# Performance work log

Measured on AMD Instinct MI355X. Metric: run time of the kernel, lower is better.

## Reference

```python
import jax, jax.numpy as jnp
import numpy as np


def setup_inputs() -> dict:
    key = jax.random.key(0)
    ks = jax.random.split(key, 5)
    B, C, S = 4, 64, 96          # batch, in_c, square spatial size
    H = 8                        # num_heads
    x = jax.random.normal(ks[0], (B, C, S, S), dtype=jnp.float32)
    # 1x1 conv weights stored as (out_c, in_c) matrices
    w_vkq = jax.random.normal(ks[1], (3 * H * C, C), dtype=jnp.float32) * 0.02
    b_vkq = jax.random.normal(ks[2], (3 * H * C,), dtype=jnp.float32) * 0.02
    w_out = jax.random.normal(ks[3], (C, C * H), dtype=jnp.float32) * 0.02
    b_out = jax.random.normal(ks[4], (C,), dtype=jnp.float32) * 0.02
    return {"x": x, "w_vkq": w_vkq, "b_vkq": b_vkq, "w_out": w_out, "b_out": b_out}


def reference(x, w_vkq, b_vkq, w_out, b_out):
    B, C, Hh, W = x.shape                       # module requires Hh == W
    H = w_vkq.shape[0] // (3 * C)               # num_heads
    # to_vkq: 1x1 conv == per-pixel matmul over channels -> (B, 3HC, Hh, W)
    vqk = jnp.einsum('bcxy,oc->boxy', x, w_vkq) + b_vkq[None, :, None, None]
    # torch .view reinterprets spatial (Hh, W) flat buffer as (W, Hh)
    vqk = vqk.reshape(B, 3, H, C, W, Hh)
    v, q, k = vqk[:, 0], vqk[:, 1], vqk[:, 2]
    # channel-wise attention: contract over the 'y' axis, keep channel dim
    h = jnp.einsum('bhcxy,bhczy->bhcxz', v, k) / (W * Hh)   # (B,H,C,W,W)
    h = jax.nn.softmax(h, axis=-1)
    h = jnp.einsum('bhcxy,bhczy->bhcxz', h, q)              # (B,H,C,W,W)
    # rearrange 'b h c x y -> b (c h) x y'  (c outer, h inner)
    h = h.transpose(0, 2, 1, 3, 4).reshape(B, C * H, W, W)
    # to_out: 1x1 conv back to in_c channels
    return jnp.einsum('bkxy,ok->boxy', h, w_out) + b_out[None, :, None, None]
```

## Files before the change

kernel.cpp:

```cpp
#include <hip/hip_runtime.h>
#include <cstdint>
#include <cstddef>

typedef float f32x4 __attribute__((ext_vector_type(4)));
typedef float f32x2 __attribute__((ext_vector_type(2)));
typedef __bf16 bf16x8 __attribute__((ext_vector_type(8)));
typedef __bf16 bf16x2 __attribute__((ext_vector_type(2)));
typedef uint32_t u32x4 __attribute__((ext_vector_type(4)));

#define TSS 9216
#define VST 9344
#define VSF 9472
#define KSB 104
#define KST 104
#define XST 72
#define WST 72
#define RSTD 68
#define EPS 68

#define FP8_SCALE 32.0f

__device__ __forceinline__ uint32_t pack2bf(float a, float b) {
  bf16x2 v = { (__bf16)a, (__bf16)b };
  return __builtin_bit_cast(uint32_t, v);
}
__device__ __forceinline__ uint32_t pack4fp8(float a, float b, float c, float d) {
  uint32_t r = __builtin_amdgcn_cvt_pk_fp8_f32(a, b, 0, false);
  return (uint32_t)__builtin_amdgcn_cvt_pk_fp8_f32(c, d, (int)r, true);
}
__device__ __forceinline__ uint2 fp8x4_to_bf16x4_ns(uint32_t v) {
  const f32x2 lo = __builtin_amdgcn_cvt_pk_f32_fp8((int)v, false);
  const f32x2 hi = __builtin_amdgcn_cvt_pk_f32_fp8((int)v, true);
  return uint2{pack2bf(lo[0], lo[1]), pack2bf(hi[0], hi[1])};
}

__global__ __launch_bounds__(256, 8) void wcvt_kernel(
    const float* __restrict__ w, uint16_t* __restrict__ wbf)
{
  const int i = blockIdx.x * 256 + threadIdx.x;
  const float4 v = ((const float4*)w)[i];
  ((uint2*)wbf)[i] = uint2{pack2bf(v.x * FP8_SCALE, v.y * FP8_SCALE),
                           pack2bf(v.z * FP8_SCALE, v.w * FP8_SCALE)};
}

__global__ __launch_bounds__(256, 4) void proj_kernel(
    const float* __restrict__ x, const uint16_t* __restrict__ wbf,
    const float* __restrict__ b_vkq,
    uint8_t* __restrict__ Vr, uint8_t* __restrict__ Qr, uint8_t* __restrict__ Kr)
{
  __shared__ __align__(16) uint16_t Bt[64 * XST];
  __shared__ __align__(16) uint8_t  Ep[4][16 * EPS];

  const int t   = threadIdx.x;
  const int blk = blockIdx.x;
  const int oq  = (blk >> 3) & 3;
  const int bn  = (blk & 7) | ((blk >> 5) << 3);
  const int nt  = bn % 144;
  const int b   = bn / 144;
  const int n0  = nt * 64;

  {
    const float* __restrict__ xb = x + (size_t)b * 64 * TSS + n0;
    const int p  = t & 63;
    const int c0 = (t >> 6) * 16;
    float v[16];
    #pragma unroll
    for (int i = 0; i < 16; ++i) v[i] = xb[(size_t)(c0 + i) * TSS + p];
    #pragma unroll
    for (int h = 0; h < 2; ++h)
      *(uint4*)&Bt[p * XST + c0 + h*8] =
        uint4{pack2bf(v[h*8+0], v[h*8+1]), pack2bf(v[h*8+2], v[h*8+3]),
              pack2bf(v[h*8+4], v[h*8+5]), pack2bf(v[h*8+6], v[h*8+7])};
  }
  __syncthreads();

  const int L    = t & 63;
  const int w    = t >> 6;
  const int lcol = L & 15;
  const int lq   = L >> 4;

  bf16x8 af[4][2];
  #pragma unroll
  for (int tm = 0; tm < 4; ++tm)
    #pragma unroll
    for (int ks = 0; ks < 2; ++ks)
      af[tm][ks] = *(const bf16x8*)&Bt[(tm*16 + lcol) * XST + ks*32 + lq*8];

  const int obase = oq * 384 + w * 96;

  bf16x8 bw[3][2];
  float  bias_r[3];
  #pragma unroll
  for (int pre = 0; pre < 3; ++pre) {
    const int o = obase + pre*16 + lcol;
    #pragma unroll
    for (int ks = 0; ks < 2; ++ks)
      bw[pre][ks] = *(const bf16x8*)(wbf + (size_t)o * 64 + ks*32 + lq*8);
    bias_r[pre] = b_vkq[o] * FP8_SCALE;
  }

  uint8_t* __restrict__ ep = Ep[w];

  #pragma unroll
  for (int ot = 0; ot < 6; ++ot) {
    const int s3   = ot % 3;
    const float bias = bias_r[s3];
    f32x4 acc[4];
    #pragma unroll
    for (int tm = 0; tm < 4; ++tm) acc[tm] = f32x4{bias, bias, bias, bias};
    #pragma unroll
    for (int tm = 0; tm < 4; ++tm)
      #pragma unroll
      for (int ks = 0; ks < 2; ++ks)
        acc[tm] = __builtin_amdgcn_mfma_f32_16x16x32_bf16(af[tm][ks], bw[s3][ks], acc[tm], 0, 0, 0);
    if (ot < 3) {
      const int on = obase + (ot + 3)*16 + lcol;
      #pragma unroll
      for (int ks = 0; ks < 2; ++ks)
        bw[s3][ks] = *(const bf16x8*)(wbf + (size_t)on * 64 + ks*32 + lq*8);
      bias_r[s3] = b_vkq[on] * FP8_SCALE;
    }
    #pragma unroll
    for (int tm = 0; tm < 4; ++tm)
      *(uint32_t*)&ep[lcol * EPS + tm*16 + lq*4] =
        pack4fp8(acc[tm][0], acc[tm][1], acc[tm][2], acc[tm][3]);

    const int o_t  = obase + ot * 16;
    const int sreg = o_t >> 9;
    uint8_t* __restrict__ reg = (sreg == 0) ? Vr : ((sreg == 1) ? Qr : Kr);
    const size_t rb = (size_t)(b * 512 + (o_t & 511)) * VSF + n0;
    #pragma unroll
    for (int s = 0; s < 4; ++s) {
      const int orow = s*4 + lq;
      const uint32_t d = *(const uint32_t*)&ep[orow * EPS + lcol*4];
      *(uint32_t*)(reg + rb + (size_t)orow * VSF + lcol*4) = d;
    }
  }
}

__global__ __launch_bounds__(384, 4) void attn_kernel(
    const uint8_t* __restrict__ Vr, const uint8_t* __restrict__ Qr,
    const uint8_t* __restrict__ Kr, uint16_t* __restrict__ Obuf)
{
  __shared__ __align__(16) uint8_t  KP[96 * 208];
  __shared__ __align__(16) uint16_t Qs[96 * KST];

  const int t   = threadIdx.x;
  const int blk = blockIdx.x;
  const int b   = blk >> 9;
  const int hc  = blk & 511;
  const size_t pb8 = (size_t)(b * 512 + hc) * VSF;
  const uint8_t* __restrict__ vplane = Vr + pb8;

  {
    const uint4* __restrict__ sk = (const uint4*)(Kr + pb8);
    const uint4* __restrict__ sq = (const uint4*)(Qr + pb8);
    #pragma unroll
    for (int half = 0; half < 2; ++half) {
      const int g = t + half * 384;
      if (half == 0 || t < 192) {
        const int row = g / 6, seg = g % 6;
        *(uint4*)&KP[row * KSB + seg * 16] = sk[g];
        const uint4 q4 = sq[g];
        const uint2 qa = fp8x4_to_bf16x4_ns(q4.x);
        const uint2 qb = fp8x4_to_bf16x4_ns(q4.y);
        const uint2 qc = fp8x4_to_bf16x4_ns(q4.z);
        const uint2 qd = fp8x4_to_bf16x4_ns(q4.w);
        uint16_t* d = &Qs[row * KST + seg * 16];
        *(uint4*)(d + 0) = uint4{qa.x, qa.y, qb.x, qb.y};
        *(uint4*)(d + 8) = uint4{qc.x, qc.y, qd.x, qd.y};
      }
    }
  }

  const int L    = t & 63;
  const int w    = t / 64;
  const int lcol = L & 15;
  const int lq   = L >> 4;
  const int xrow = 16 * w + lcol;
  const float C  = 1.44269504088896f / (9216.0f * (FP8_SCALE * FP8_SCALE));
  const f32x4 zero4 = {0.f, 0.f, 0.f, 0.f};

  long bv[3];
  #pragma unroll
  for (int ks = 0; ks < 3; ++ks)
    bv[ks] = *(const long*)(vplane + (size_t)xrow * 96 + ks*32 + lq*8);

  __syncthreads();

  f32x4 sa[6];
  #pragma unroll
  for (int i = 0; i < 6; ++i) sa[i] = zero4;
  #pragma unroll
  for (int tz = 0; tz < 6; ++tz)
    #pragma unroll
    for (int ks = 0; ks < 3; ++ks) {
      const long ak = *(const long*)&KP[(tz*16 + lcol) * KSB + ks*32 + lq*8];
      sa[tz] = __builtin_amdgcn_mfma_f32_16x16x32_fp8_fp8(ak, bv[ks], sa[tz], 0, 0, 0);
    }

  float s = 0.f;
  #pragma unroll
  for (int tz = 0; tz < 6; ++tz)
    #pragma unroll
    for (int r = 0; r < 4; ++r) {
      const float e = __builtin_exp2f(sa[tz][r] * C);
      sa[tz][r] = e;
      s += e;
    }
  s += __shfl_xor(s, 16, 64);
  s += __shfl_xor(s, 32, 64);
  const float inv = 1.0f / (s * FP8_SCALE);

  __syncthreads();

  uint16_t* __restrict__ Ps = (uint16_t*)KP;
  #pragma unroll
  for (int tz = 0; tz < 6; ++tz) {
    const float p0 = sa[tz][0] * inv;
    const float p1 = sa[tz][1] * inv;
    const float p2 = sa[tz][2] * inv;
    const float p3 = sa[tz][3] * inv;
    *(uint2*)&Ps[xrow * KST + tz*16 + lq*4] = uint2{pack2bf(p0, p1), pack2bf(p2, p3)};
  }

  bf16x8 bp[3];
  #pragma unroll
  for (int ks = 0; ks < 3; ++ks)
    bp[ks] = *(const bf16x8*)&Ps[xrow * KST + ks*32 + lq*8];
  f32x4 oa[6];
  #pragma unroll
  for (int i = 0; i < 6; ++i) oa[i] = zero4;
  #pragma unroll
  for (int tz = 0; tz < 6; ++tz)
    #pragma unroll
    for (int ks = 0; ks < 3; ++ks) {
      const bf16x8 aq = *(const bf16x8*)&Qs[(tz*16 + lcol) * KST + ks*32 + lq*8];
      oa[tz] = __builtin_amdgcn_mfma_f32_16x16x32_bf16(aq, bp[ks], oa[tz], 0, 0, 0);
    }

  uint16_t* __restrict__ dst = Obuf + (size_t)(b * 512 + hc) * VST;
  #pragma unroll
  for (int tz = 0; tz < 6; ++tz)
    *(uint2*)(dst + (size_t)xrow * 96 + tz*16 + lq*4) =
      uint2{pack2bf(oa[tz][0], oa[tz][1]), pack2bf(oa[tz][2], oa[tz][3])};
}

__global__ __launch_bounds__(256, 4) void out_proj_kernel(
    const uint16_t* __restrict__ Obuf, const float* __restrict__ w_out,
    const float* __restrict__ b_out, float* __restrict__ out)
{
  __shared__ __align__(16) uint32_t As2[2][32 * RSTD];
  __shared__ __align__(16) uint16_t Wl[2][64 * WST];

  const int t    = threadIdx.x;
  const int blk  = blockIdx.x;
  const int nt   = blk % 144;
  const int b    = blk / 144;
  const int n0   = nt * 64;
  const int L    = t & 63;
  const int w    = t >> 6;
  const int lcol = L & 15;
  const int lq   = L >> 4;
  const int kp_g = t >> 4;
  const int seg  = t & 15;

  const uint16_t* __restrict__ ab = Obuf + (size_t)b * 512 * VST;

  uint2  pa[2][2];
  float4 pw[4];

  auto load_chunk = [&](int k0) {
    #pragma unroll
    for (int i = 0; i < 2; ++i) {
      const int kp = kp_g + i * 16;
      const int ke = k0 + 2*kp, ko = ke + 1;
      const int pe = ((ke & 7) << 6) | (ke >> 3);
      const int po = ((ko & 7) << 6) | (ko >> 3);
      pa[i][0] = *(const uint2*)(ab + (size_t)pe * VST + n0 + seg * 4);
      pa[i][1] = *(const uint2*)(ab + (size_t)po * VST + n0 + seg * 4);
    }
    #pragma unroll
    for (int i = 0; i < 4; ++i) {
      const int idx = t + i * 256;
      pw[i] = *(const float4*)(w_out + (size_t)(idx >> 4) * 512 + k0 + (idx & 15) * 4);
    }
  };

  auto store_chunk = [&](int buf) {
    #pragma unroll
    for (int i = 0; i < 2; ++i) {
      const int kp = kp_g + i * 16;
      const uint2 a = pa[i][0], bb = pa[i][1];
      uint4 d;
      d.x = (a.x & 0xffffu) | (bb.x << 16);
      d.y = (a.x >> 16)     | (bb.x & 0xffff0000u);
      d.z = (a.y & 0xffffu) | (bb.y << 16);
      d.w = (a.y >> 16)     | (bb.y & 0xffff0000u);
      *(uint4*)&As2[buf][kp * RSTD + seg * 4] = d;
    }
    #pragma unroll
    for (int i = 0; i < 4; ++i) {
      const int idx = t + i * 256;
      const float4 v = pw[i];
      *(uint2*)&Wl[buf][(idx >> 4) * WST + (idx & 15) * 4] =
        uint2{pack2bf(v.x, v.y), pack2bf(v.z, v.w)};
    }
  };

  f32x4 acc[4];
  const f32x4 zero4 = {0.f, 0.f, 0.f, 0.f};
  #pragma unroll
  for (int tm = 0; tm < 4; ++tm) acc[tm] = zero4;

  load_chunk(0);

  for (int c = 0; c < 8; ++c) {
    const int buf = c & 1;
    store_chunk(buf);
    if (c < 7) load_chunk((c + 1) * 64);
    __syncthreads();
    #pragma unroll
    for (int ks = 0; ks < 2; ++ks) {
      u32x4 bb;
      #pragma unroll
      for (int jj = 0; jj < 4; ++jj)
        bb[jj] = As2[buf][(ks*16 + lq*4 + jj) * RSTD + w*16 + lcol];
      const bf16x8 bfr = __builtin_bit_cast(bf16x8, bb);
      #pragma unroll
      for (int tm = 0; tm < 4; ++tm) {
        const bf16x8 af = *(const bf16x8*)&Wl[buf][(tm*16 + lcol) * WST + ks*32 + lq*8];
        acc[tm] = __builtin_amdgcn_mfma_f32_16x16x32_bf16(af, bfr, acc[tm], 0, 0, 0);
      }
    }
  }

  const int p = n0 + w*16 + lcol;
  #pragma unroll
  for (int tm = 0; tm < 4; ++tm)
    #pragma unroll
    for (int r = 0; r < 4; ++r) {
      const int o = tm*16 + lq*4 + r;
      out[(size_t)(b * 64 + o) * TSS + p] = acc[tm][r] + b_out[o];
    }
}

extern "C" void kernel_launch(void* const* d_in, const int* in_sizes, int n_in,
                              void* d_out, int out_size, void* d_ws, size_t ws_size,
                              hipStream_t stream) {
  const float* x     = (const float*)d_in[0];
  const float* w_vkq = (const float*)d_in[1];
  const float* b_vkq = (const float*)d_in[2];
  const float* w_out = (const float*)d_in[3];
  const float* b_out = (const float*)d_in[4];
  float* out = (float*)d_out;

  uint16_t* Obuf = (uint16_t*)d_ws;
  uint8_t*  Vr   = (uint8_t*)(Obuf + (size_t)2048 * VST);
  uint8_t*  Qr   = Vr + (size_t)2048 * VSF;
  uint8_t*  Kr   = Qr + (size_t)2048 * VSF;
  uint16_t* wbf  = (uint16_t*)(Kr + (size_t)2048 * VSF);

  wcvt_kernel<<<dim3(96), dim3(256), 0, stream>>>(w_vkq, wbf);
  proj_kernel<<<dim3(2304), dim3(256), 0, stream>>>(x, wbf, b_vkq, Vr, Qr, Kr);
  attn_kernel<<<dim3(2048), dim3(384), 0, stream>>>(Vr, Qr, Kr, Obuf);
  out_proj_kernel<<<dim3(576), dim3(256), 0, stream>>>(Obuf, w_out, b_out, out);
}
```

Baseline: 122.5 us.

## Drop weight-convert kernel, widen proj stores, halve out-proj tile width

Removes the separate wcvt kernel. proj_kernel now reads fp32 w_vkq directly and converts it to bf16 in registers, and the FP8 scale is applied to x instead of to the weights. The proj epilogue stores 8-byte chunks instead of 4-byte ones. out_proj_kernel switches to 32-pixel tiles with a 2x2 warp split, doubling the grid to 1152 blocks for more parallelism. It also adds a trailing __syncthreads per chunk, and the scaling change may alter bf16 rounding slightly.

```diff
diff --git a/kernel.cpp b/kernel.cpp
--- a/kernel.cpp
+++ b/kernel.cpp
@@ -15,7 +15,7 @@
 #define KST 104
 #define XST 72
 #define WST 72
-#define RSTD 68
+#define RST2 36
 #define EPS 68
 
 #define FP8_SCALE 32.0f
@@ -33,18 +33,16 @@
   const f32x2 hi = __builtin_amdgcn_cvt_pk_f32_fp8((int)v, true);
   return uint2{pack2bf(lo[0], lo[1]), pack2bf(hi[0], hi[1])};
 }
-
-__global__ __launch_bounds__(256, 8) void wcvt_kernel(
-    const float* __restrict__ w, uint16_t* __restrict__ wbf)
-{
-  const int i = blockIdx.x * 256 + threadIdx.x;
-  const float4 v = ((const float4*)w)[i];
-  ((uint2*)wbf)[i] = uint2{pack2bf(v.x * FP8_SCALE, v.y * FP8_SCALE),
-                           pack2bf(v.z * FP8_SCALE, v.w * FP8_SCALE)};
+__device__ __forceinline__ bf16x8 ld_w8(const float* __restrict__ p) {
+  const float4 a = *(const float4*)p;
+  const float4 b = *(const float4*)(p + 4);
+  const uint4 r = uint4{pack2bf(a.x, a.y), pack2bf(a.z, a.w),
+                        pack2bf(b.x, b.y), pack2bf(b.z, b.w)};
+  return __builtin_bit_cast(bf16x8, r);
 }
 
 __global__ __launch_bounds__(256, 4) void proj_kernel(
-    const float* __restrict__ x, const uint16_t* __restrict__ wbf,
+    const float* __restrict__ x, const float* __restrict__ w_vkq,
     const float* __restrict__ b_vkq,
     uint8_t* __restrict__ Vr, uint8_t* __restrict__ Qr, uint8_t* __restrict__ Kr)
 {
@@ -65,7 +63,7 @@
     const int c0 = (t >> 6) * 16;
     float v[16];
     #pragma unroll
-    for (int i = 0; i < 16; ++i) v[i] = xb[(size_t)(c0 + i) * TSS + p];
+    for (int i = 0; i < 16; ++i) v[i] = xb[(size_t)(c0 + i) * TSS + p] * FP8_SCALE;
     #pragma unroll
     for (int h = 0; h < 2; ++h)
       *(uint4*)&Bt[p * XST + c0 + h*8] =
@@ -95,11 +93,13 @@
     const int o = obase + pre*16 + lcol;
     #pragma unroll
     for (int ks = 0; ks < 2; ++ks)
-      bw[pre][ks] = *(const bf16x8*)(wbf + (size_t)o * 64 + ks*32 + lq*8);
+      bw[pre][ks] = ld_w8(w_vkq + (size_t)o * 64 + ks*32 + lq*8);
     bias_r[pre] = b_vkq[o] * FP8_SCALE;
   }
 
   uint8_t* __restrict__ ep = Ep[w];
+  const int r8 = L >> 3;
+  const int c8 = L & 7;
 
   #pragma unroll
   for (int ot = 0; ot < 6; ++ot) {
@@ -117,7 +117,7 @@
       const int on = obase + (ot + 3)*16 + lcol;
       #pragma unroll
       for (int ks = 0; ks < 2; ++ks)
-        bw[s3][ks] = *(const bf16x8*)(wbf + (size_t)on * 64 + ks*32 + lq*8);
+        bw[s3][ks] = ld_w8(w_vkq + (size_t)on * 64 + ks*32 + lq*8);
       bias_r[s3] = b_vkq[on] * FP8_SCALE;
     }
     #pragma unroll
@@ -130,10 +130,10 @@
     uint8_t* __restrict__ reg = (sreg == 0) ? Vr : ((sreg == 1) ? Qr : Kr);
     const size_t rb = (size_t)(b * 512 + (o_t & 511)) * VSF + n0;
     #pragma unroll
-    for (int s = 0; s < 4; ++s) {
-      const int orow = s*4 + lq;
-      const uint32_t d = *(const uint32_t*)&ep[orow * EPS + lcol*4];
-      *(uint32_t*)(reg + rb + (size_t)orow * VSF + lcol*4) = d;
+    for (int s = 0; s < 2; ++s) {
+      const int orow = s*8 + r8;
+      const uint2 d2 = *(const uint2*)&ep[orow * EPS + c8*8];
+      *(uint2*)(reg + rb + (size_t)orow * VSF + c8*8) = d2;
     }
   }
 }
@@ -250,36 +250,34 @@
     const uint16_t* __restrict__ Obuf, const float* __restrict__ w_out,
     const float* __restrict__ b_out, float* __restrict__ out)
 {
-  __shared__ __align__(16) uint32_t As2[2][32 * RSTD];
+  __shared__ __align__(16) uint32_t As2[2][32 * RST2];
   __shared__ __align__(16) uint16_t Wl[2][64 * WST];
 
   const int t    = threadIdx.x;
   const int blk  = blockIdx.x;
-  const int nt   = blk % 144;
-  const int b    = blk / 144;
-  const int n0   = nt * 64;
+  const int nt   = blk % 288;
+  const int b    = blk / 288;
+  const int n0   = nt * 32;
   const int L    = t & 63;
   const int w    = t >> 6;
+  const int wp   = w & 1;
+  const int wo   = w >> 1;
   const int lcol = L & 15;
   const int lq   = L >> 4;
-  const int kp_g = t >> 4;
-  const int seg  = t & 15;
+  const int kp_g = t >> 3;
+  const int seg  = t & 7;
 
   const uint16_t* __restrict__ ab = Obuf + (size_t)b * 512 * VST;
 
-  uint2  pa[2][2];
+  uint2  pa[2];
   float4 pw[4];
 
   auto load_chunk = [&](int k0) {
-    #pragma unroll
-    for (int i = 0; i < 2; ++i) {
-      const int kp = kp_g + i * 16;
-      const int ke = k0 + 2*kp, ko = ke + 1;
-      const int pe = ((ke & 7) << 6) | (ke >> 3);
-      const int po = ((ko & 7) << 6) | (ko >> 3);
-      pa[i][0] = *(const uint2*)(ab + (size_t)pe * VST + n0 + seg * 4);
-      pa[i][1] = *(const uint2*)(ab + (size_t)po * VST + n0 + seg * 4);
-    }
+    const int ke = k0 + 2*kp_g, ko = ke + 1;
+    const int pe = ((ke & 7) << 6) | (ke >> 3);
+    const int po = ((ko & 7) << 6) | (ko >> 3);
+    pa[0] = *(const uint2*)(ab + (size_t)pe * VST + n0 + seg * 4);
+    pa[1] = *(const uint2*)(ab + (size_t)po * VST + n0 + seg * 4);
     #pragma unroll
     for (int i = 0; i < 4; ++i) {
       const int idx = t + i * 256;
@@ -288,16 +286,14 @@
   };
 
   auto store_chunk = [&](int buf) {
-    #pragma unroll
-    for (int i = 0; i < 2; ++i) {
-      const int kp = kp_g + i * 16;
-      const uint2 a = pa[i][0], bb = pa[i][1];
+    {
+      const uint2 a = pa[0], bb = pa[1];
       uint4 d;
       d.x = (a.x & 0xffffu) | (bb.x << 16);
       d.y = (a.x >> 16)     | (bb.x & 0xffff0000u);
       d.z = (a.y & 0xffffu) | (bb.y << 16);
       d.w = (a.y >> 16)     | (bb.y & 0xffff0000u);
-      *(uint4*)&As2[buf][kp * RSTD + seg * 4] = d;
+      *(uint4*)&As2[buf][kp_g * RST2 + seg * 4] = d;
     }
     #pragma unroll
     for (int i = 0; i < 4; ++i) {
@@ -308,10 +304,10 @@
     }
   };
 
-  f32x4 acc[4];
+  f32x4 acc[2];
   const f32x4 zero4 = {0.f, 0.f, 0.f, 0.f};
   #pragma unroll
-  for (int tm = 0; tm < 4; ++tm) acc[tm] = zero4;
+  for (int tm = 0; tm < 2; ++tm) acc[tm] = zero4;
 
   load_chunk(0);
 
@@ -325,22 +321,23 @@
       u32x4 bb;
       #pragma unroll
       for (int jj = 0; jj < 4; ++jj)
-        bb[jj] = As2[buf][(ks*16 + lq*4 + jj) * RSTD + w*16 + lcol];
+        bb[jj] = As2[buf][(ks*16 + lq*4 + jj) * RST2 + wp*16 + lcol];
       const bf16x8 bfr = __builtin_bit_cast(bf16x8, bb);
       #pragma unroll
-      for (int tm = 0; tm < 4; ++tm) {
-        const bf16x8 af = *(const bf16x8*)&Wl[buf][(tm*16 + lcol) * WST + ks*32 + lq*8];
+      for (int tm = 0; tm < 2; ++tm) {
+        const bf16x8 af = *(const bf16x8*)&Wl[buf][((wo*2 + tm)*16 + lcol) * WST + ks*32 + lq*8];
         acc[tm] = __builtin_amdgcn_mfma_f32_16x16x32_bf16(af, bfr, acc[tm], 0, 0, 0);
       }
     }
-  }
-
-  const int p = n0 + w*16 + lcol;
-  #pragma unroll
-  for (int tm = 0; tm < 4; ++tm)
+    __syncthreads();
+  }
+
+  const int p = n0 + wp*16 + lcol;
+  #pragma unroll
+  for (int tm = 0; tm < 2; ++tm)
     #pragma unroll
     for (int r = 0; r < 4; ++r) {
-      const int o = tm*16 + lq*4 + r;
+      const int o = wo*32 + tm*16 + lq*4 + r;
       out[(size_t)(b * 64 + o) * TSS + p] = acc[tm][r] + b_out[o];
     }
 }
@@ -359,10 +356,8 @@
   uint8_t*  Vr   = (uint8_t*)(Obuf + (size_t)2048 * VST);
   uint8_t*  Qr   = Vr + (size_t)2048 * VSF;
   uint8_t*  Kr   = Qr + (size_t)2048 * VSF;
-  uint16_t* wbf  = (uint16_t*)(Kr + (size_t)2048 * VSF);
-
-  wcvt_kernel<<<dim3(96), dim3(256), 0, stream>>>(w_vkq, wbf);
-  proj_kernel<<<dim3(2304), dim3(256), 0, stream>>>(x, wbf, b_vkq, Vr, Qr, Kr);
+
+  proj_kernel<<<dim3(2304), dim3(256), 0, stream>>>(x, w_vkq, b_vkq, Vr, Qr, Kr);
   attn_kernel<<<dim3(2048), dim3(384), 0, stream>>>(Vr, Qr, Kr, Obuf);
-  out_proj_kernel<<<dim3(576), dim3(256), 0, stream>>>(Obuf, w_out, b_out, out);
-}
+  out_proj_kernel<<<dim3(1152), dim3(256), 0, stream>>>(Obuf, w_out, b_out, out);
+}
```

Result: slower. 133.8 us (+9.2%).
